# Performance work log

Measured on AMD Instinct MI355X. Metric: run time of the kernel, lower is better.

Reference implementation:

```python
import jax, jax.numpy as jnp
import numpy as np

B = 512          # graphs
NODES = 90       # nodes per graph (fixed by lin1 = Linear(90*L*H, ...))
N = B * NODES    # total nodes
F_IN = 90        # dataset.num_features
H = 128          # hidden
L = 3            # num_layers
HL = 64          # hidden_linear
C = 2            # dataset.num_classes
DEG = 16         # avg degree
E = N * DEG      # total edges


def setup_inputs() -> dict:
    key = jax.random.key(0)
    ks = jax.random.split(key, 14)
    x = jax.random.normal(ks[0], (N, F_IN), jnp.float32)
    # intra-graph random edges: graph g owns nodes [g*90, (g+1)*90)
    g = jnp.repeat(jnp.arange(B), NODES * DEG)
    src = g * NODES + jax.random.randint(ks[1], (E,), 0, NODES)
    dst = g * NODES + jax.random.randint(ks[2], (E,), 0, NODES)
    edge_index = jnp.stack([src, dst]).astype(jnp.int64)
    edge_attr = jax.random.uniform(ks[3], (E,), jnp.float32, 0.1, 1.0)
    batch = jnp.repeat(jnp.arange(B), NODES).astype(jnp.int64)

    def lin(k, fi, fo):
        s = 1.0 / np.sqrt(fi)
        kw, kb = jax.random.split(k)
        return (jax.random.uniform(kw, (fi, fo), jnp.float32, -s, s),
                jax.random.uniform(kb, (fo,), jnp.float32, -s, s))

    W1, b1 = lin(ks[4], F_IN, H)
    W2, b2 = lin(ks[5], H, H)
    W3, b3 = lin(ks[6], H, H)
    lin1_W, lin1_b = lin(ks[7], NODES * L * H, HL)
    lin2_W, lin2_b = lin(ks[8], HL, C)
    return {"x": x, "edge_attr": edge_attr, "W1": W1, "b1": b1, "W2": W2,
            "b2": b2, "W3": W3, "b3": b3, "lin1_W": lin1_W, "lin1_b": lin1_b,
            "lin2_W": lin2_W, "lin2_b": lin2_b, "edge_index": edge_index,
            "batch": batch}


def reference(x, edge_attr, W1, b1, W2, b2, W3, b3, lin1_W, lin1_b,
              lin2_W, lin2_b, edge_index, batch):
    src, dst = edge_index[0], edge_index[1]
    # GCN normalization with added self-loops (weight 1), as in PyG GCNConv
    loop = jnp.arange(N)
    s = jnp.concatenate([src, loop])
    d = jnp.concatenate([dst, loop])
    w = jnp.concatenate([edge_attr, jnp.ones((N,), x.dtype)])
    deg = jax.ops.segment_sum(w, d, num_segments=N)
    dis = jnp.where(deg > 0, jax.lax.rsqrt(jnp.maximum(deg, 1e-30)), 0.0)
    norm = dis[s] * w * dis[d]  # [E+N]

    def conv(h, W, b):
        h = h @ W                                  # [N, H]
        msg = norm[:, None] * h[s]                 # gather+scale [E+N, H]
        return jax.ops.segment_sum(msg, d, num_segments=N) + b

    h1 = jax.nn.relu(conv(x, W1, b1))
    h2 = jax.nn.relu(conv(h1, W2, b2))
    h3 = jax.nn.relu(conv(h2, W3, b3))
    xc = jnp.concatenate([h1, h2, h3], axis=1)     # [N, L*H]
    # to_dense_batch: every graph has exactly 90 nodes in order, so no padding
    # (fill_value never appears) and dense batching is a pure reshape.
    z = xc.reshape(B, NODES * L * H)
    h = jax.nn.relu(z @ lin1_W + lin1_b)
    logits = h @ lin2_W + lin2_b                   # dropout is identity in eval
    return jax.nn.log_softmax(logits, axis=-1)
```

## Files before the change

kernel.cpp:

```cpp
#include <hip/hip_runtime.h>

typedef __bf16 bfx8 __attribute__((ext_vector_type(8)));
typedef float fx4 __attribute__((ext_vector_type(4)));
typedef unsigned short us4 __attribute__((ext_vector_type(4)));
typedef unsigned short us8 __attribute__((ext_vector_type(8)));

#define NNODES 90
#define NPAD   96
#define HF     128
#define NGRAPH 512
#define EPG    1440
#define ETOT   (NGRAPH*EPG)
#define KTOT   34560
#define NKTOT  1080
#define KSPLIT 45
#define KSTEPS (NKTOT/KSPLIT)

__device__ __forceinline__ unsigned short f2bf(float f){
  union { float f; unsigned u; } v; v.f = f;
  return (unsigned short)((v.u + 0x7FFFu + ((v.u>>16)&1u)) >> 16);
}
__device__ __forceinline__ int hsw(int node, int f){
  return node*HF + ((((f>>3) ^ (node&15)))<<3) + (f&7);
}

__global__ __launch_bounds__(256) void pack_all_kern(
    const float* __restrict__ W1,
    const float* __restrict__ W2,
    const float* __restrict__ W3,
    const float* __restrict__ L1W,
    unsigned short* __restrict__ o1,
    unsigned short* __restrict__ o2,
    unsigned short* __restrict__ o3,
    unsigned short* __restrict__ l1p)
{
  __shared__ __align__(16) unsigned short tile[32*64];
  int b = blockIdx.x;
  int t = threadIdx.x;
  if (b < NKTOT) {
    int ks = b;
#pragma unroll
    for (int j=0;j<8;j++) tile[t*8+j] = f2bf(L1W[ks*32*64 + t*8 + j]);
    __syncthreads();
    int lane = t & 63;
    int nt = t >> 6;
    int n  = nt*16 + (lane&15);
    int kq = (lane>>4)*8;
    us8 v;
#pragma unroll
    for (int j=0;j<8;j++) v[j] = tile[(kq+j)*64 + n];
    *(us8*)&l1p[((nt*NKTOT + ks)*64 + lane)*8] = v;
  } else {
    int bb = b - NKTOT;
    const float* W; unsigned short* out; int K, nK, tt;
    if (bb < 6)       { W = W1; out = o1; K = 90;  nK = 3; tt = bb*256 + t; }
    else if (bb < 14) { W = W2; out = o2; K = 128; nK = 4; tt = (bb-6)*256 + t; }
    else              { W = W3; out = o3; K = 128; nK = 4; tt = (bb-14)*256 + t; }
    int lane = tt & 63;
    int ks = (tt>>6) % nK;
    int nt = (tt>>6) / nK;
    int n  = nt*16 + (lane&15);
    int k0 = ks*32 + (lane>>4)*8;
    unsigned short v[8];
#pragma unroll
    for (int j=0;j<8;j++){ int k=k0+j; v[j] = (k<K)? f2bf(W[k*128+n]) : (unsigned short)0; }
    unsigned short* o = out + ((nt*nK+ks)*64 + lane)*8;
#pragma unroll
    for (int j=0;j<8;j++) o[j]=v[j];
  }
}

__global__ __launch_bounds__(512) void gcn_layers_kern(
    const float* __restrict__ x,
    const float* __restrict__ eattr,
    const int* __restrict__ ei,
    const unsigned short* __restrict__ w1p,
    const unsigned short* __restrict__ w2p,
    const unsigned short* __restrict__ w3p,
    const float* __restrict__ b1,
    const float* __restrict__ b2,
    const float* __restrict__ b3,
    unsigned short* __restrict__ xc)
{
  __shared__ __align__(16) char smem[65280];
  unsigned short* Abf = (unsigned short*)smem;
  unsigned short* H   = (unsigned short*)(smem + 17280);
  unsigned short* Tt  = (unsigned short*)(smem + 40320);
  float* Af  = (float*)(smem + 17280);
  float* deg = (float*)(smem + 64896);

  const int g = blockIdx.x;
  const int tid = threadIdx.x;
  const int lane = tid & 63, wave = tid >> 6;
  const int q = lane >> 4, r = lane & 15;
  const int eb = g*EPG;
  const int nb = g*NNODES;
  const long long* e64 = (const long long*)ei;

  bool i64f;
  {
    int v = ei[2*lane + 1];
    i64f = (__ballot(v != 0) == 0ull);
  }

  const int e0 = tid, e1 = tid + 512, e2 = tid + 1024;
  const bool h2 = (e2 < EPG);
  int s0, d0, s1, d1, s2 = nb, d2 = nb;
  if (i64f) {
    s0 = (int)e64[eb+e0]; d0 = (int)e64[ETOT+eb+e0];
    s1 = (int)e64[eb+e1]; d1 = (int)e64[ETOT+eb+e1];
    if (h2) { s2 = (int)e64[eb+e2]; d2 = (int)e64[ETOT+eb+e2]; }
  } else {
    s0 = ei[eb+e0]; d0 = ei[ETOT+eb+e0];
    s1 = ei[eb+e1]; d1 = ei[ETOT+eb+e1];
    if (h2) { s2 = ei[eb+e2]; d2 = ei[ETOT+eb+e2]; }
  }
  float w0 = eattr[eb+e0];
  float w1 = eattr[eb+e1];
  float w2 = h2 ? eattr[eb+e2] : 0.f;

  for (int i = tid*4; i < NNODES*NPAD; i += 512*4) {
    fx4 zv = {0.f,0.f,0.f,0.f};
    *(fx4*)&Af[i] = zv;
  }
  __syncthreads();
  atomicAdd(&Af[(d0-nb)*NPAD + (s0-nb)], w0);
  atomicAdd(&Af[(d1-nb)*NPAD + (s1-nb)], w1);
  if (h2) atomicAdd(&Af[(d2-nb)*NPAD + (s2-nb)], w2);
  __syncthreads();
  {
    int l16 = tid & 15;
    for (int row = tid >> 4; row < NPAD; row += 32) {
      float s = 0.f;
      if (row < NNODES) {
#pragma unroll
        for (int j = 0; j < 6; ++j) s += Af[row*NPAD + l16 + 16*j];
      }
      s += __shfl_xor(s, 1);
      s += __shfl_xor(s, 2);
      s += __shfl_xor(s, 4);
      s += __shfl_xor(s, 8);
      if (l16 == 0) deg[row] = (row < NNODES) ? rsqrtf(1.f + s) : 1.0f;
    }
  }
  __syncthreads();
  for (int i = tid; i < NNODES*NPAD; i += 512) {
    int row = i / NPAD, col = i - row*NPAD;
    float a = Af[i];
    if (col == row) a += 1.0f;
    Abf[i] = f2bf(a * deg[row] * deg[col]);
  }
  __syncthreads();
  for (int i = tid; i < NNODES*90; i += 512) {
    int node = i/90, f = i - node*90;
    H[hsw(node, f)] = f2bf(x[(nb + node)*90 + f]);
  }
  for (int i = tid; i < NNODES*6; i += 512) {
    int node = i/6, f = 90 + (i - node*6);
    H[hsw(node, f)] = 0;
  }
  __syncthreads();

#pragma unroll
  for (int l = 0; l < 3; ++l) {
    const unsigned short* wpk = (l==0)? w1p : (l==1)? w2p : w3p;
    const float* bias         = (l==0)? b1 : (l==1)? b2 : b3;
    const int nK = (l==0)? 3 : 4;

    bfx8 wf[4];
#pragma unroll
    for (int ks = 0; ks < 4; ++ks)
      if (ks < nK) wf[ks] = *(const bfx8*)(const void*)&wpk[((wave*nK + ks)*64 + lane)*8];

    for (int mt = 0; mt < 6; ++mt) {
      int row = mt*16 + r; if (row > 89) row = 89;
      fx4 acc = {0.f,0.f,0.f,0.f};
#pragma unroll
      for (int ks = 0; ks < 4; ++ks)
        if (ks < nK) {
          bfx8 af = *(const bfx8*)(const void*)&H[row*HF + (((4*ks + q) ^ (row&15))<<3)];
          acc = __builtin_amdgcn_mfma_f32_16x16x32_bf16(af, wf[ks], acc, 0,0,0);
        }
      us4 o;
#pragma unroll
      for (int i2=0;i2<4;i2++) o[i2] = f2bf(acc[i2]);
      *(us4*)&Tt[(wave*16 + r)*NPAD + mt*16 + q*4] = o;
    }
    __syncthreads();

    {
      bfx8 tf[3];
#pragma unroll
      for (int ks = 0; ks < 3; ++ks)
        tf[ks] = *(const bfx8*)(const void*)&Tt[(wave*16 + r)*NPAD + ks*32 + q*8];
      float bv[4];
#pragma unroll
      for (int i2=0;i2<4;i2++) bv[i2] = bias[wave*16 + q*4 + i2];
      for (int nt = 0; nt < 6; ++nt) {
        int arow = nt*16 + r; if (arow > 89) arow = 89;
        fx4 acc = {0.f,0.f,0.f,0.f};
#pragma unroll
        for (int ks = 0; ks < 3; ++ks) {
          bfx8 bfr = *(const bfx8*)(const void*)&Abf[arow*NPAD + ks*32 + q*8];
          acc = __builtin_amdgcn_mfma_f32_16x16x32_bf16(tf[ks], bfr, acc, 0,0,0);
        }
        int m = nt*16 + r;
        if (m < NNODES) {
          us4 o;
#pragma unroll
          for (int i2=0;i2<4;i2++){
            float v = acc[i2] + bv[i2];
            o[i2] = f2bf(v > 0.f ? v : 0.f);
          }
          *(us4*)&H[m*HF + (((2*wave + (q>>1)) ^ (m&15))<<3) + (q&1)*4] = o;
        }
      }
    }
    __syncthreads();

    for (int i = tid*8; i < NNODES*HF; i += 512*8) {
      int node = i >> 7, p = (i >> 3) & 15;
      us8 v = *(const us8*)&H[i];
      int f0 = (p ^ (node&15)) << 3;
      *(us8*)&xc[(nb + node)*384 + l*128 + f0] = v;
    }
  }
}

__global__ __launch_bounds__(256) void gemm2_kern(
    const unsigned short* __restrict__ z,
    const unsigned short* __restrict__ wp,
    float* __restrict__ pbuf)
{
  int mb = blockIdx.x % 8;
  int kb = blockIdx.x / 8;
  int tid = threadIdx.x;
  int lane = tid & 63, wave = tid >> 6;
  int q = lane >> 4, r = lane & 15;
  int m0 = mb*64;

  const unsigned short* zbase = &z[(m0 + wave*16 + r)*KTOT + (kb*KSTEPS)*32 + q*8];
  const unsigned short* wb = &wp[(kb*KSTEPS)*512 + lane*8];

  fx4 acc[4] = {{0,0,0,0},{0,0,0,0},{0,0,0,0},{0,0,0,0}};
#pragma unroll 4
  for (int it = 0; it < KSTEPS; ++it) {
    bfx8 af = *(const bfx8*)(const void*)&zbase[it*32];
#pragma unroll
    for (int nt = 0; nt < 4; ++nt) {
      bfx8 bf = *(const bfx8*)(const void*)&wb[(nt*NKTOT + it)*512];
      acc[nt] = __builtin_amdgcn_mfma_f32_16x16x32_bf16(af, bf, acc[nt], 0,0,0);
    }
  }
  float* pb = &pbuf[(kb*NGRAPH + m0 + wave*16)*64];
#pragma unroll
  for (int nt = 0; nt < 4; ++nt)
#pragma unroll
    for (int i2 = 0; i2 < 4; ++i2)
      pb[(q*4 + i2)*64 + nt*16 + r] = acc[nt][i2];
}

__global__ __launch_bounds__(256) void head_kern(
    const float* __restrict__ pbuf,
    const float* __restrict__ l1b,
    const float* __restrict__ l2w,
    const float* __restrict__ l2b,
    float* __restrict__ out)
{
  int gph = blockIdx.x*4 + (threadIdx.x >> 6);
  int j = threadIdx.x & 63;
  float h = l1b[j];
  for (int kb = 0; kb < KSPLIT; ++kb)
    h += pbuf[(kb*NGRAPH + gph)*64 + j];
  h = h > 0.f ? h : 0.f;
  float p0 = h * l2w[2*j];
  float p1 = h * l2w[2*j+1];
  for (int off = 32; off; off >>= 1) {
    p0 += __shfl_down(p0, off);
    p1 += __shfl_down(p1, off);
  }
  if (j == 0) {
    float l0 = p0 + l2b[0];
    float l1 = p1 + l2b[1];
    float mx = fmaxf(l0, l1);
    float lse = mx + logf(expf(l0-mx) + expf(l1-mx));
    out[gph*2]   = l0 - lse;
    out[gph*2+1] = l1 - lse;
  }
}

extern "C" void kernel_launch(void* const* d_in, const int* in_sizes, int n_in,
                              void* d_out, int out_size, void* d_ws, size_t ws_size,
                              hipStream_t stream)
{
  const float* x   = (const float*)d_in[0];
  const float* ea  = (const float*)d_in[1];
  const float* W1  = (const float*)d_in[2];
  const float* b1  = (const float*)d_in[3];
  const float* W2  = (const float*)d_in[4];
  const float* b2  = (const float*)d_in[5];
  const float* W3  = (const float*)d_in[6];
  const float* b3  = (const float*)d_in[7];
  const float* L1W = (const float*)d_in[8];
  const float* L1b = (const float*)d_in[9];
  const float* L2W = (const float*)d_in[10];
  const float* L2b = (const float*)d_in[11];
  const int* ei    = (const int*)d_in[12];
  float* out       = (float*)d_out;

  char* ws = (char*)d_ws;
  unsigned short* xc  = (unsigned short*)(ws);
  unsigned short* l1p = (unsigned short*)(ws + 35389440);
  unsigned short* w1p = (unsigned short*)(ws + 39813120);
  unsigned short* w2p = (unsigned short*)(ws + 39837696);
  unsigned short* w3p = (unsigned short*)(ws + 39870464);
  float* pbuf         = (float*)(ws + 39903232);

  pack_all_kern<<<NKTOT + 22, 256, 0, stream>>>(W1, W2, W3, L1W,
                                                w1p, w2p, w3p, l1p);
  gcn_layers_kern<<<NGRAPH, 512, 0, stream>>>(x, ea, ei, w1p, w2p, w3p,
                                              b1, b2, b3, xc);
  gemm2_kern<<<8*KSPLIT, 256, 0, stream>>>(xc, l1p, pbuf);
  head_kern<<<NGRAPH/4, 256, 0, stream>>>(pbuf, L1b, L2W, L2b, out);
}
```

Measured before the change: 145.2 us.

## Vectorize weight packing, prefetch x early, write layer outputs directly to xc

The pack kernel now loads lin1 weights as float4 vectors and stores bf16 pairs to shared memory as vector stores instead of scalar loops. The GCN kernel prefetches the node features into registers before the edge loads so their latency overlaps the adjacency build. Each layer's output is written straight from the MFMA epilogue to the global xc buffer, which removes a barrier and an LDS copy-out loop per layer and skips the LDS write for the last layer. The trade-off is smaller, scattered 8-byte global stores instead of 16-byte coalesced ones, plus 16 extra registers for the prefetched features.

```diff
diff --git a/kernel.cpp b/kernel.cpp
--- a/kernel.cpp
+++ b/kernel.cpp
@@ -39,8 +39,13 @@
   int t = threadIdx.x;
   if (b < NKTOT) {
     int ks = b;
-#pragma unroll
-    for (int j=0;j<8;j++) tile[t*8+j] = f2bf(L1W[ks*32*64 + t*8 + j]);
+    fx4 a0 = *(const fx4*)&L1W[ks*2048 + t*8];
+    fx4 a1 = *(const fx4*)&L1W[ks*2048 + t*8 + 4];
+    us4 c0, c1;
+#pragma unroll
+    for (int j=0;j<4;j++){ c0[j] = f2bf(a0[j]); c1[j] = f2bf(a1[j]); }
+    *(us4*)&tile[t*8]     = c0;
+    *(us4*)&tile[t*8 + 4] = c1;
     __syncthreads();
     int lane = t & 63;
     int nt = t >> 6;
@@ -103,6 +108,13 @@
     i64f = (__ballot(v != 0) == 0ull);
   }
 
+  float xr[16];
+#pragma unroll
+  for (int k = 0; k < 16; ++k) {
+    int i = tid + k*512;
+    xr[k] = (i < NNODES*90) ? x[nb*90 + i] : 0.f;
+  }
+
   const int e0 = tid, e1 = tid + 512, e2 = tid + 1024;
   const bool h2 = (e2 < EPG);
   int s0, d0, s1, d1, s2 = nb, d2 = nb;
@@ -151,9 +163,13 @@
     Abf[i] = f2bf(a * deg[row] * deg[col]);
   }
   __syncthreads();
-  for (int i = tid; i < NNODES*90; i += 512) {
-    int node = i/90, f = i - node*90;
-    H[hsw(node, f)] = f2bf(x[(nb + node)*90 + f]);
+#pragma unroll
+  for (int k = 0; k < 16; ++k) {
+    int i = tid + k*512;
+    if (i < NNODES*90) {
+      int node = i/90, f = i - node*90;
+      H[hsw(node, f)] = f2bf(xr[k]);
+    }
   }
   for (int i = tid; i < NNODES*6; i += 512) {
     int node = i/6, f = 90 + (i - node*6);
@@ -212,18 +228,14 @@
             float v = acc[i2] + bv[i2];
             o[i2] = f2bf(v > 0.f ? v : 0.f);
           }
-          *(us4*)&H[m*HF + (((2*wave + (q>>1)) ^ (m&15))<<3) + (q&1)*4] = o;
+          *(us4*)&xc[(nb + m)*384 + l*128 + wave*16 + q*4] = o;
+          if (l < 2) {
+            *(us4*)&H[m*HF + (((2*wave + (q>>1)) ^ (m&15))<<3) + (q&1)*4] = o;
+          }
         }
       }
     }
-    __syncthreads();
-
-    for (int i = tid*8; i < NNODES*HF; i += 512*8) {
-      int node = i >> 7, p = (i >> 3) & 15;
-      us8 v = *(const us8*)&H[i];
-      int f0 = (p ^ (node&15)) << 3;
-      *(us8*)&xc[(nb + node)*384 + l*128 + f0] = v;
-    }
+    if (l < 2) __syncthreads();
   }
 }
 
```

After: 147.7 us. Within noise of the previous version (+1.7%).
